# Kernel tuning notes

Hardware: AMD Instinct MI355X
Metric: run time of the kernel (lower is better)

The kernel has to match this reference:

```python
import jax, jax.numpy as jnp
import numpy as np

NUM_HEADS = 8
NUM_GROUPS = 32  # min(C//4, 32) for C=512
EPS = 1e-6       # flax GroupNorm default


def setup_inputs() -> dict:
    key = jax.random.key(0)
    ks = jax.random.split(key, 3)
    B, H, W, D, C = 2, 16, 16, 16, 512
    x = jax.random.normal(ks[0], (B, H, W, D, C), dtype=jnp.float32)
    w_qkv = jax.random.normal(ks[1], (C, 3 * C), dtype=jnp.float32) / np.sqrt(C)
    w_proj = jax.random.normal(ks[2], (C, C), dtype=jnp.float32) / np.sqrt(C)
    return {
        "x": x,
        "gn_scale": jnp.ones((C,), jnp.float32),
        "gn_bias": jnp.zeros((C,), jnp.float32),
        "w_qkv": w_qkv,
        "b_qkv": jnp.zeros((3 * C,), jnp.float32),
        "w_proj": w_proj,
        "b_proj": jnp.zeros((C,), jnp.float32),
    }


def group_norm(x, scale, bias):
    # x: [B, S, C]; normalize within each of NUM_GROUPS channel groups over (S, group-channels)
    B, S, C = x.shape
    xg = x.reshape(B, S, NUM_GROUPS, C // NUM_GROUPS)
    mean = jnp.mean(xg, axis=(1, 3), keepdims=True)
    var = jnp.var(xg, axis=(1, 3), keepdims=True)
    xn = (xg - mean) * jax.lax.rsqrt(var + EPS)
    return xn.reshape(B, S, C) * scale + bias


def reference(x, gn_scale, gn_bias, w_qkv, b_qkv, w_proj, b_proj):
    B, H, W, D, C = x.shape
    S = H * W * D
    hd = C // NUM_HEADS
    xf = x.reshape(B, S, C)
    q_in = group_norm(xf, gn_scale, gn_bias)
    # 1x1x1 conv == per-position dense
    qkv = q_in @ w_qkv + b_qkv                      # [B, S, 3C]
    qkv = qkv.reshape(B, S, NUM_HEADS, 3 * hd)
    q, k, v = jnp.split(qkv, 3, axis=-1)            # each [B, S, nh, hd]
    scale = 1.0 / jnp.sqrt(jnp.asarray(hd, x.dtype))
    logits = jnp.einsum('btnh,bfnh->bnft', k, q * scale)  # [B, nh, S, S]
    weights = jax.nn.softmax(logits, axis=-1)
    h = jnp.einsum('bnft,btnh->bfnh', weights, v)   # [B, S, nh, hd]
    h = h.reshape(B, S, C) @ w_proj + b_proj
    return h.reshape(x.shape) + x
```

## Files before the change

### kernel.cpp

```cpp
#include <hip/hip_runtime.h>

typedef __attribute__((ext_vector_type(8))) short short8;
typedef __attribute__((ext_vector_type(4))) float f32x4;
typedef __attribute__((ext_vector_type(16))) float f32x16;

#define S_LEN 4096
#define C_DIM 512
#define NH 8
#define HD 64
#define NG 32
#define GS 16
#define LOG2E 1.44269504088896340736f

__device__ __forceinline__ unsigned short f2bf(float f) {
  union { float f; unsigned int u; } v; v.f = f;
  unsigned int r = v.u + 0x7fffu + ((v.u >> 16) & 1u);
  return (unsigned short)(r >> 16);
}

__device__ __forceinline__ float bf2f(unsigned short s) {
  union { unsigned u; float f; } v; v.u = (unsigned)s << 16;
  return v.f;
}

__device__ __forceinline__ float fexp2(float x) {
  float r;
  asm("v_exp_f32 %0, %1" : "=v"(r) : "v"(x));
  return r;
}

__device__ __forceinline__ unsigned pk_bf16(float a, float b) {
  unsigned r;
  asm("v_cvt_pk_bf16_f32 %0, %1, %2" : "=v"(r) : "v"(a), "v"(b));
  return r;
}

__device__ __forceinline__ void pl_swap(unsigned& a, unsigned& b) {
  asm("v_permlane32_swap_b32 %0, %1" : "+v"(a), "+v"(b));
}

__device__ __forceinline__ void gload_lds16(const void* g, void* l) {
  __builtin_amdgcn_global_load_lds((const __attribute__((address_space(1))) void*)g,
                                   (__attribute__((address_space(3))) void*)l, 16, 0, 0);
}

__global__ __launch_bounds__(256) void prep_kernel(const float* __restrict__ x,
                                                   float* __restrict__ partials,
                                                   const float* __restrict__ w_qkv,
                                                   unsigned short* __restrict__ wqkvT,
                                                   const float* __restrict__ w_proj,
                                                   unsigned short* __restrict__ wprojT) {
  __shared__ float tile[32][33];
  __shared__ float r1[4], r2[4];
  int bid = blockIdx.x;
  if (bid < 256) {
    int bg = bid >> 2, chunk = bid & 3;
    int b = bg >> 5, g = bg & 31;
    const float* xp = x + (size_t)b * S_LEN * C_DIM + g * GS;
    float s1 = 0.f, s2 = 0.f;
    for (int i = threadIdx.x; i < 1024 * 4; i += 256) {
      int s = chunk * 1024 + (i >> 2), c4 = i & 3;
      float4 v = *(const float4*)&xp[(size_t)s * C_DIM + c4 * 4];
      s1 += v.x + v.y + v.z + v.w;
      s2 += v.x * v.x + v.y * v.y + v.z * v.z + v.w * v.w;
    }
    for (int off = 1; off < 64; off <<= 1) {
      s1 += __shfl_xor(s1, off);
      s2 += __shfl_xor(s2, off);
    }
    int w = threadIdx.x >> 6;
    if ((threadIdx.x & 63) == 0) { r1[w] = s1; r2[w] = s2; }
    __syncthreads();
    if (threadIdx.x == 0) {
      partials[bg * 8 + chunk * 2]     = r1[0] + r1[1] + r1[2] + r1[3];
      partials[bg * 8 + chunk * 2 + 1] = r2[0] + r2[1] + r2[2] + r2[3];
    }
    return;
  }
  const float* src; unsigned short* dst; int K, N, n0, k0;
  if (bid < 1024) {
    int t = bid - 256;  src = w_qkv;  dst = wqkvT;  K = 512; N = 1536;
    n0 = (t % 48) * 32; k0 = (t / 48) * 32;
  } else {
    int t = bid - 1024; src = w_proj; dst = wprojT; K = 512; N = 512;
    n0 = (t % 16) * 32; k0 = (t / 16) * 32;
  }
  int c = threadIdx.x & 31, r0 = threadIdx.x >> 5;
  for (int i = 0; i < 4; ++i) {
    int r = r0 + i * 8;
    tile[r][c] = src[(size_t)(k0 + r) * N + n0 + c];
  }
  __syncthreads();
  for (int i = 0; i < 4; ++i) {
    int r = r0 + i * 8;
    dst[(size_t)(n0 + r) * K + k0 + c] = f2bf(tile[c][r]);
  }
}

__global__ __launch_bounds__(256) void gn_apply_kernel(const float* __restrict__ x,
                                                       const float* __restrict__ partials,
                                                       const float* __restrict__ scale,
                                                       const float* __restrict__ bias,
                                                       unsigned short* __restrict__ out) {
  int idx = blockIdx.x * 256 + threadIdx.x;
  int e = idx * 4;
  int c = e & (C_DIM - 1);
  int bs = e >> 9;
  int b = bs >> 12;
  int grp = b * NG + (c >> 4);
  float s1 = partials[grp * 8] + partials[grp * 8 + 2] + partials[grp * 8 + 4] + partials[grp * 8 + 6];
  float s2 = partials[grp * 8 + 1] + partials[grp * 8 + 3] + partials[grp * 8 + 5] + partials[grp * 8 + 7];
  const float invN = 1.0f / (float)(S_LEN * GS);
  float mean = s1 * invN;
  float var = s2 * invN - mean * mean;
  float rstd = rsqrtf(var + 1e-6f);
  float4 v = *(const float4*)&x[e];
  ushort4 o;
  o.x = f2bf((v.x - mean) * rstd * scale[c]     + bias[c]);
  o.y = f2bf((v.y - mean) * rstd * scale[c + 1] + bias[c + 1]);
  o.z = f2bf((v.z - mean) * rstd * scale[c + 2] + bias[c + 2]);
  o.w = f2bf((v.w - mean) * rstd * scale[c + 3] + bias[c + 3]);
  *(ushort4*)&out[e] = o;
}

template <int MODE>
__global__ __launch_bounds__(256) void gemm_kernel(const unsigned short* __restrict__ A,
                                                   const unsigned short* __restrict__ Bt,
                                                   const float* __restrict__ bias,
                                                   unsigned short* __restrict__ qh,
                                                   unsigned short* __restrict__ kh,
                                                   unsigned short* __restrict__ vh,
                                                   const float* __restrict__ resid,
                                                   float* __restrict__ outf,
                                                   int K) {
  __shared__ unsigned short Alds[128][72];
  __shared__ unsigned short Blds[128][72];
  int tid = threadIdx.x, lane = tid & 63, w = tid >> 6;
  int li = lane & 15, g = lane >> 4;
  int wr = (w >> 1) * 64, wc = (w & 1) * 64;
  int m0 = blockIdx.y * 128, n0 = blockIdx.x * 128;
  f32x4 acc[4][4];
  for (int i = 0; i < 4; ++i)
    for (int j = 0; j < 4; ++j) acc[i][j] = (f32x4){0.f, 0.f, 0.f, 0.f};

  for (int k0 = 0; k0 < K; k0 += 64) {
    for (int i = 0; i < 4; ++i) {
      int ch = tid + i * 256;
      int r = ch >> 3, c8 = (ch & 7) * 8;
      *(int4*)&Alds[r][c8] = *(const int4*)&A[(size_t)(m0 + r) * K + k0 + c8];
      *(int4*)&Blds[r][c8] = *(const int4*)&Bt[(size_t)(n0 + r) * K + k0 + c8];
    }
    __syncthreads();
    for (int ks = 0; ks < 2; ++ks) {
      short8 af[4], bfm[4];
      for (int mi = 0; mi < 4; ++mi)
        af[mi] = *(const short8*)&Alds[wr + mi * 16 + li][ks * 32 + g * 8];
      for (int ni = 0; ni < 4; ++ni)
        bfm[ni] = *(const short8*)&Blds[wc + ni * 16 + li][ks * 32 + g * 8];
      for (int mi = 0; mi < 4; ++mi)
        for (int ni = 0; ni < 4; ++ni)
          acc[mi][ni] = __builtin_amdgcn_mfma_f32_16x16x32_bf16(af[mi], bfm[ni], acc[mi][ni], 0, 0, 0);
    }
    __syncthreads();
  }

  if (MODE == 0) {
    for (int ni = 0; ni < 4; ++ni) {
      int n = n0 + wc + ni * 16 + li;
      float bn = bias[n];
      int head = n / 192;
      int rem = n - head * 192;
      int part = rem >> 6;
      int h = rem & 63;
      unsigned short* dst = part == 0 ? qh : (part == 1 ? kh : vh);
      float mul = part == 0 ? 0.125f * LOG2E : 1.0f;
      for (int mi = 0; mi < 4; ++mi)
        for (int j = 0; j < 4; ++j) {
          int m = m0 + wr + mi * 16 + g * 4 + j;
          int b = m >> 12, s = m & 4095;
          float val = (acc[mi][ni][j] + bn) * mul;
          size_t idx;
          if (part == 2) idx = ((size_t)(b * NH + head) * HD + h) * S_LEN + s;
          else           idx = ((size_t)(b * NH + head) * S_LEN + s) * HD + h;
          dst[idx] = f2bf(val);
        }
    }
  } else {
    for (int ni = 0; ni < 4; ++ni) {
      int n = n0 + wc + ni * 16 + li;
      float bn = bias[n];
      for (int mi = 0; mi < 4; ++mi)
        for (int j = 0; j < 4; ++j) {
          int m = m0 + wr + mi * 16 + g * 4 + j;
          size_t off = (size_t)m * C_DIM + n;
          outf[off] = acc[mi][ni][j] + bn + resid[off];
        }
    }
  }
}

template <int SPLIT>
__global__ __launch_bounds__(256, 4) void attn_kernel(const unsigned short* __restrict__ qh,
                                                      const unsigned short* __restrict__ kh,
                                                      const unsigned short* __restrict__ vt,
                                                      unsigned short* __restrict__ ob,
                                                      unsigned short* __restrict__ opart,
                                                      float* __restrict__ lpart) {
  __shared__ unsigned char Kt[3 * 4096];
  __shared__ unsigned char Vt[3 * 4096];
  int bn = blockIdx.y;
  int half = SPLIT > 1 ? blockIdx.z : 0;
  int tid = threadIdx.x, lane = tid & 63, wv = tid >> 6;
  int r32 = lane & 31, hi_ = lane >> 5;
  int q0 = blockIdx.x * 128 + wv * 32;
  const int NT = S_LEN / 32 / SPLIT;
  const unsigned short* qp = qh + (size_t)bn * S_LEN * HD;
  const char* kp = (const char*)(kh + (size_t)bn * S_LEN * HD);
  const char* vp = (const char*)(vt + (size_t)bn * HD * S_LEN);

  int srow  = wv * 8 + (lane >> 3);
  int scolS = (lane & 7) * 16;
  int sc    = scolS ^ ((srow & 7) << 4);
  const char* kSrc = kp + (size_t)srow * 128 + sc + (size_t)half * (S_LEN / SPLIT) * 128;
  int vh_ = srow + ((sc >> 6) << 5);
  const char* vSrc = vp + (size_t)vh_ * (S_LEN * 2) + (sc & 63) + (size_t)half * (S_LEN / SPLIT) * 2;

  short8 qf[4];
#pragma unroll
  for (int ks = 0; ks < 4; ++ks)
    qf[ks] = *(const short8*)&qp[(size_t)(q0 + r32) * HD + ks * 16 + hi_ * 8];

  union { unsigned u[4]; short8 v; } ones;
#pragma unroll
  for (int i = 0; i < 4; ++i) ones.u[i] = 0x3F803F80u;

  f32x16 o0, o1, lacc, z16;
#pragma unroll
  for (int i = 0; i < 16; ++i) { o0[i] = 0.f; o1[i] = 0.f; lacc[i] = 0.f; z16[i] = 0.f; }

  int swzr = (r32 & 7) << 4;
  int sBase = wv * 1024;

  gload_lds16(kSrc, &Kt[sBase]);
  gload_lds16(vSrc, &Vt[sBase]);
  gload_lds16(kSrc + 32 * 128, &Kt[4096 + sBase]);
  gload_lds16(vSrc + 32 * 2,   &Vt[4096 + sBase]);
  asm volatile("s_waitcnt vmcnt(2)" ::: "memory");
  __builtin_amdgcn_s_barrier();

  int curO = 0, nxtO = 4096, nnO = 8192;
  for (int it = 0; it < NT; ++it) {
    bool more = (it + 2 < NT);
    if (more) {
      size_t t0n = (size_t)(it + 2) * 32;
      gload_lds16(kSrc + t0n * 128, &Kt[nnO + sBase]);
      gload_lds16(vSrc + t0n * 2,   &Vt[nnO + sBase]);
    }

    const unsigned char* Kr = &Kt[curO + r32 * 128];
    const unsigned char* Vr = &Vt[curO + r32 * 128];
    short8 kf[4], vf[4];
#pragma unroll
    for (int ks = 0; ks < 4; ++ks)
      kf[ks] = *(const short8*)&Kr[(ks * 32 + hi_ * 16) ^ swzr];
#pragma unroll
    for (int kk = 0; kk < 2; ++kk)
#pragma unroll
      for (int hf = 0; hf < 2; ++hf)
        vf[kk * 2 + hf] = *(const short8*)&Vr[(hf * 64 + kk * 32 + hi_ * 16) ^ swzr];

    f32x16 s = __builtin_amdgcn_mfma_f32_32x32x16_bf16(kf[0], qf[0], z16, 0, 0, 0);
#pragma unroll
    for (int ks = 1; ks < 4; ++ks)
      s = __builtin_amdgcn_mfma_f32_32x32x16_bf16(kf[ks], qf[ks], s, 0, 0, 0);

#pragma unroll
    for (int i = 0; i < 16; ++i) s[i] = fexp2(s[i]);

    unsigned pkv[8];
#pragma unroll
    for (int g2 = 0; g2 < 8; ++g2) pkv[g2] = pk_bf16(s[2 * g2], s[2 * g2 + 1]);
    pl_swap(pkv[0], pkv[2]); pl_swap(pkv[1], pkv[3]);
    pl_swap(pkv[4], pkv[6]); pl_swap(pkv[5], pkv[7]);
    union { unsigned u[4]; short8 v; } F0, F1;
    F0.u[0] = pkv[0]; F0.u[1] = pkv[1]; F0.u[2] = pkv[2]; F0.u[3] = pkv[3];
    F1.u[0] = pkv[4]; F1.u[1] = pkv[5]; F1.u[2] = pkv[6]; F1.u[3] = pkv[7];

    o0 = __builtin_amdgcn_mfma_f32_32x32x16_bf16(vf[0], F0.v, o0, 0, 0, 0);
    o1 = __builtin_amdgcn_mfma_f32_32x32x16_bf16(vf[1], F0.v, o1, 0, 0, 0);
    lacc = __builtin_amdgcn_mfma_f32_32x32x16_bf16(ones.v, F0.v, lacc, 0, 0, 0);
    o0 = __builtin_amdgcn_mfma_f32_32x32x16_bf16(vf[2], F1.v, o0, 0, 0, 0);
    o1 = __builtin_amdgcn_mfma_f32_32x32x16_bf16(vf[3], F1.v, o1, 0, 0, 0);
    lacc = __builtin_amdgcn_mfma_f32_32x32x16_bf16(ones.v, F1.v, lacc, 0, 0, 0);

    if (more) asm volatile("s_waitcnt vmcnt(2)" ::: "memory");
    else      asm volatile("s_waitcnt vmcnt(0)" ::: "memory");
    __builtin_amdgcn_s_barrier();
    int t = curO; curO = nxtO; nxtO = nnO; nnO = t;
  }

  if (SPLIT == 1) {
    float inv = 1.0f / lacc[0];
    int b = bn >> 3, n = bn & 7;
    size_t base = ((size_t)(b * S_LEN + q0 + r32)) * C_DIM + n * HD;
#pragma unroll
    for (int r = 0; r < 16; ++r) {
      int hrow = (r & 3) + 8 * (r >> 2) + 4 * hi_;
      ob[base + hrow]      = f2bf(o0[r] * inv);
      ob[base + 32 + hrow] = f2bf(o1[r] * inv);
    }
  } else {
    size_t row = (size_t)(bn * SPLIT + half) * S_LEN + q0 + r32;
    unsigned short* pp = opart + row * 64;
#pragma unroll
    for (int i = 0; i < 8; ++i) {
      int r = 2 * i;
      int hrow = (r & 3) + 8 * (r >> 2) + 4 * hi_;
      *(unsigned*)&pp[hrow]      = pk_bf16(o0[r], o0[r + 1]);
      *(unsigned*)&pp[32 + hrow] = pk_bf16(o1[r], o1[r + 1]);
    }
    if (!hi_) lpart[row] = lacc[0];
  }
}

template <int SPLIT>
__global__ __launch_bounds__(256) void attn_combine_kernel(const unsigned short* __restrict__ opart,
                                                           const float* __restrict__ lpart,
                                                           unsigned short* __restrict__ ob) {
  int idx = blockIdx.x * 256 + threadIdx.x;
  int h0 = (idx & 7) * 8;
  int q  = (idx >> 3) & (S_LEN - 1);
  int bn = idx >> 15;
  float acc[8];
#pragma unroll
  for (int j = 0; j < 8; ++j) acc[j] = 0.f;
  float lsum = 0.f;
#pragma unroll
  for (int z = 0; z < SPLIT; ++z) {
    size_t row = (size_t)(bn * SPLIT + z) * S_LEN + q;
    lsum += lpart[row];
    short8 a = *(const short8*)&opart[row * 64 + h0];
#pragma unroll
    for (int j = 0; j < 8; ++j) acc[j] += bf2f((unsigned short)a[j]);
  }
  float inv = 1.0f / lsum;
  union { unsigned short us[8]; short8 v; } R;
#pragma unroll
  for (int j = 0; j < 8; ++j) R.us[j] = f2bf(acc[j] * inv);
  int b_ = bn >> 3, n = bn & 7;
  *(short8*)&ob[((size_t)(b_ * S_LEN + q)) * C_DIM + n * HD + h0] = R.v;
}

extern "C" void kernel_launch(void* const* d_in, const int* in_sizes, int n_in,
                              void* d_out, int out_size, void* d_ws, size_t ws_size,
                              hipStream_t stream) {
  const float* x        = (const float*)d_in[0];
  const float* gn_scale = (const float*)d_in[1];
  const float* gn_bias  = (const float*)d_in[2];
  const float* w_qkv    = (const float*)d_in[3];
  const float* b_qkv    = (const float*)d_in[4];
  const float* w_proj   = (const float*)d_in[5];
  const float* b_proj   = (const float*)d_in[6];
  float* out = (float*)d_out;

  char* ws = (char*)d_ws;
  unsigned short* q_in   = (unsigned short*)(ws);
  unsigned short* wqkvT  = (unsigned short*)(ws + 8388608);
  unsigned short* wprojT = (unsigned short*)(ws + 9961472);
  unsigned short* qhb    = (unsigned short*)(ws + 10485760);
  unsigned short* khb    = (unsigned short*)(ws + 18874368);
  unsigned short* vtb    = (unsigned short*)(ws + 27262976);
  unsigned short* ahb    = (unsigned short*)(ws + 35651584);
  float* partials        = (float*)(ws + 44040192);
  float* lpart           = (float*)(ws + 44042240);
  unsigned short* opart  = (unsigned short*)(ws + 45090816);
  const size_t NEED2 = 45090816ull + (size_t)16 * 2 * S_LEN * 64 * 2;
  const size_t NEED4 = 45090816ull + (size_t)16 * 4 * S_LEN * 64 * 2;

  prep_kernel<<<1280, 256, 0, stream>>>(x, partials, w_qkv, wqkvT, w_proj, wprojT);
  gn_apply_kernel<<<4096, 256, 0, stream>>>(x, partials, gn_scale, gn_bias, q_in);
  gemm_kernel<0><<<dim3(12, 64), 256, 0, stream>>>(q_in, wqkvT, b_qkv, qhb, khb, vtb, nullptr, nullptr, 512);
  if (ws_size >= NEED4) {
    attn_kernel<4><<<dim3(32, 16, 4), 256, 0, stream>>>(qhb, khb, vtb, ahb, opart, lpart);
    attn_combine_kernel<4><<<2048, 256, 0, stream>>>(opart, lpart, ahb);
  } else if (ws_size >= NEED2) {
    attn_kernel<2><<<dim3(32, 16, 2), 256, 0, stream>>>(qhb, khb, vtb, ahb, opart, lpart);
    attn_combine_kernel<2><<<2048, 256, 0, stream>>>(opart, lpart, ahb);
  } else {
    attn_kernel<1><<<dim3(32, 16, 1), 256, 0, stream>>>(qhb, khb, vtb, ahb, nullptr, nullptr);
  }
  gemm_kernel<1><<<dim3(4, 64), 256, 0, stream>>>(ahb, wprojT, b_proj, nullptr, nullptr, nullptr, x, out, 512);
}
```

Measured before the change: 161.1 us.

## Use direct global-to-LDS loads with XOR swizzle in GEMM; drop 4-way attention split

The GEMM kernel now stages A and B tiles with direct global-to-LDS 16-byte loads into an XOR-swizzled unpadded layout, replacing register-staged copies into padded arrays, and fully unrolls the inner loops. K is hardcoded to 512. Separately, the 4-way KV split attention path is removed so the 2-way split is used even when workspace allows 4. This aims to cut VGPR traffic and LDS bank conflicts in the GEMMs, at the cost of less attention parallelism.

```diff
diff --git a/kernel.cpp b/kernel.cpp
--- a/kernel.cpp
+++ b/kernel.cpp
@@ -131,33 +131,49 @@
                                                    unsigned short* __restrict__ kh,
                                                    unsigned short* __restrict__ vh,
                                                    const float* __restrict__ resid,
-                                                   float* __restrict__ outf,
-                                                   int K) {
-  __shared__ unsigned short Alds[128][72];
-  __shared__ unsigned short Blds[128][72];
+                                                   float* __restrict__ outf) {
+  __shared__ unsigned char Alds[16384];
+  __shared__ unsigned char Blds[16384];
   int tid = threadIdx.x, lane = tid & 63, w = tid >> 6;
   int li = lane & 15, g = lane >> 4;
   int wr = (w >> 1) * 64, wc = (w & 1) * 64;
   int m0 = blockIdx.y * 128, n0 = blockIdx.x * 128;
+
+  int srow = tid >> 3;
+  int colS = (tid & 7) * 16;
+  int sc   = colS ^ ((srow & 7) << 4);
+  const char* aSrc = (const char*)A + (size_t)(m0 + srow) * 1024 + sc;
+  const char* bSrc = (const char*)Bt + (size_t)(n0 + srow) * 1024 + sc;
+
   f32x4 acc[4][4];
   for (int i = 0; i < 4; ++i)
     for (int j = 0; j < 4; ++j) acc[i][j] = (f32x4){0.f, 0.f, 0.f, 0.f};
 
-  for (int k0 = 0; k0 < K; k0 += 64) {
-    for (int i = 0; i < 4; ++i) {
-      int ch = tid + i * 256;
-      int r = ch >> 3, c8 = (ch & 7) * 8;
-      *(int4*)&Alds[r][c8] = *(const int4*)&A[(size_t)(m0 + r) * K + k0 + c8];
-      *(int4*)&Blds[r][c8] = *(const int4*)&Bt[(size_t)(n0 + r) * K + k0 + c8];
-    }
-    __syncthreads();
+  for (int k0 = 0; k0 < 512; k0 += 64) {
+#pragma unroll
+    for (int r = 0; r < 4; ++r) {
+      gload_lds16(aSrc + (size_t)r * 32 * 1024 + k0 * 2, &Alds[r * 4096 + tid * 16]);
+      gload_lds16(bSrc + (size_t)r * 32 * 1024 + k0 * 2, &Blds[r * 4096 + tid * 16]);
+    }
+    asm volatile("s_waitcnt vmcnt(0)" ::: "memory");
+    __builtin_amdgcn_s_barrier();
+
+#pragma unroll
     for (int ks = 0; ks < 2; ++ks) {
       short8 af[4], bfm[4];
+#pragma unroll
+      for (int mi = 0; mi < 4; ++mi) {
+        int row = wr + mi * 16 + li;
+        af[mi] = *(const short8*)&Alds[row * 128 + ((ks * 64 + g * 16) ^ ((row & 7) << 4))];
+      }
+#pragma unroll
+      for (int ni = 0; ni < 4; ++ni) {
+        int row = wc + ni * 16 + li;
+        bfm[ni] = *(const short8*)&Blds[row * 128 + ((ks * 64 + g * 16) ^ ((row & 7) << 4))];
+      }
+#pragma unroll
       for (int mi = 0; mi < 4; ++mi)
-        af[mi] = *(const short8*)&Alds[wr + mi * 16 + li][ks * 32 + g * 8];
-      for (int ni = 0; ni < 4; ++ni)
-        bfm[ni] = *(const short8*)&Blds[wc + ni * 16 + li][ks * 32 + g * 8];
-      for (int mi = 0; mi < 4; ++mi)
+#pragma unroll
         for (int ni = 0; ni < 4; ++ni)
           acc[mi][ni] = __builtin_amdgcn_mfma_f32_16x16x32_bf16(af[mi], bfm[ni], acc[mi][ni], 0, 0, 0);
     }
@@ -375,19 +391,15 @@
   float* lpart           = (float*)(ws + 44042240);
   unsigned short* opart  = (unsigned short*)(ws + 45090816);
   const size_t NEED2 = 45090816ull + (size_t)16 * 2 * S_LEN * 64 * 2;
-  const size_t NEED4 = 45090816ull + (size_t)16 * 4 * S_LEN * 64 * 2;
 
   prep_kernel<<<1280, 256, 0, stream>>>(x, partials, w_qkv, wqkvT, w_proj, wprojT);
   gn_apply_kernel<<<4096, 256, 0, stream>>>(x, partials, gn_scale, gn_bias, q_in);
-  gemm_kernel<0><<<dim3(12, 64), 256, 0, stream>>>(q_in, wqkvT, b_qkv, qhb, khb, vtb, nullptr, nullptr, 512);
-  if (ws_size >= NEED4) {
-    attn_kernel<4><<<dim3(32, 16, 4), 256, 0, stream>>>(qhb, khb, vtb, ahb, opart, lpart);
-    attn_combine_kernel<4><<<2048, 256, 0, stream>>>(opart, lpart, ahb);
-  } else if (ws_size >= NEED2) {
+  gemm_kernel<0><<<dim3(12, 64), 256, 0, stream>>>(q_in, wqkvT, b_qkv, qhb, khb, vtb, nullptr, nullptr);
+  if (ws_size >= NEED2) {
     attn_kernel<2><<<dim3(32, 16, 2), 256, 0, stream>>>(qhb, khb, vtb, ahb, opart, lpart);
     attn_combine_kernel<2><<<2048, 256, 0, stream>>>(opart, lpart, ahb);
   } else {
     attn_kernel<1><<<dim3(32, 16, 1), 256, 0, stream>>>(qhb, khb, vtb, ahb, nullptr, nullptr);
   }
-  gemm_kernel<1><<<dim3(4, 64), 256, 0, stream>>>(ahb, wprojT, b_proj, nullptr, nullptr, nullptr, x, out, 512);
-}
+  gemm_kernel<1><<<dim3(4, 64), 256, 0, stream>>>(ahb, wprojT, b_proj, nullptr, nullptr, nullptr, x, out);
+}
```

After: 153.5 us. -4.7%, faster.
